# Performance work log

Measured on AMD Instinct MI355X. Metric: run time of the kernel, lower is better.

## Reference

```python
import jax, jax.numpy as jnp
import numpy as np

# Config constants (match init_kwargs)
H = 1024   # hidden_size
F = 4096   # intermediate_size
E = 8      # num_moe_experts
K = 2      # moe_router_topk
S, B = 1024, 2  # seq_len, micro-batch


def setup_inputs() -> dict:
    key = jax.random.key(0)
    ks = jax.random.split(key, 6)
    return {
        "hidden_states": jax.random.normal(ks[0], (S, B, H), jnp.float32),
        "router_w": jax.random.normal(ks[1], (H, E), jnp.float32) * 0.02,
        "w1": jax.random.normal(ks[2], (E, H, F), jnp.float32) * 0.02,
        "b1": jax.random.normal(ks[3], (E, F), jnp.float32) * 0.02,
        "w2": jax.random.normal(ks[4], (E, F, H), jnp.float32) * 0.02,
        "b2": jax.random.normal(ks[5], (E, H), jnp.float32) * 0.02,
    }


def reference(hidden_states, router_w, w1, b1, w2, b2):
    S_, B_, H_ = hidden_states.shape
    x = hidden_states.reshape(-1, H_)                      # [N, H]
    N = x.shape[0]

    # --- TopKRouter (aux_loss routing): topk over logits, softmax over top-k logits ---
    logits = x @ router_w                                  # [N, E]
    top_logits, indices = jax.lax.top_k(logits, K)         # [N, K]
    scores = jax.nn.softmax(top_logits.astype(jnp.float32), axis=-1).astype(logits.dtype)

    # Combine weights [N, E]: scatter top-k scores into expert slots.
    combine = jnp.zeros((N, E), x.dtype).at[jnp.arange(N)[:, None], indices].add(scores)

    # --- Experts: per-expert GPTNeoXMLP (dense over all tokens; math-equivalent
    # to dispatch (token_permutation) + grouped GEMM + scatter_add combine
    # (token_unpermutation) with score weighting for topk>1) ---
    h = jax.nn.gelu(jnp.einsum('nh,ehf->enf', x, w1) + b1[:, None, :], approximate=False)
    y = jnp.einsum('enf,efh->enh', h, w2) + b2[:, None, :]  # [E, N, H]

    out = jnp.einsum('ne,enh->nh', combine, y)              # weighted combine
    return out.reshape(S_, B_, H_)
```

## Files before the change

kernel.cpp:

```cpp
#include <hip/hip_runtime.h>
#include <cmath>


#define H_DIM 1024
#define F_DIM 4096
#define E_NUM 8
#define N_TOK 2048
#define BK 32
#define MAX_SLOTS 5120
#define MAX_MT 40
#define G1_GRID (MAX_MT * 32)
#define G2_GRID (MAX_MT * 8 * 2)
#define CVT_BLKS 2048
#define WCHUNKS (E_NUM * H_DIM * F_DIM / 8)
#define XCHUNKS (N_TOK * H_DIM / 8)

typedef short s16x4 __attribute__((ext_vector_type(4)));
typedef short s16x8 __attribute__((ext_vector_type(8)));
typedef float f32x4 __attribute__((ext_vector_type(4)));
typedef __attribute__((address_space(3))) const unsigned short* lds_us;

__device__ __forceinline__ unsigned short f2bf(float f) {
  unsigned int u = __float_as_uint(f);
  u += 0x7fffu + ((u >> 16) & 1u);
  return (unsigned short)(u >> 16);
}

__device__ __forceinline__ void gload_lds16(const void* g, void* l) {
  __builtin_amdgcn_global_load_lds(
      (const __attribute__((address_space(1))) unsigned int*)g,
      (__attribute__((address_space(3))) unsigned int*)l, 16, 0, 0);
}

__device__ __forceinline__ int xcd_swz(int orig, int nwg) {
  const int cpx = nwg >> 3;
  return (orig & 7) * cpx + (orig >> 3);
}

__device__ __forceinline__ float fast_gelu(float v) {
  const float w = v * (1.0f + 0.044715f * v * v);
  const float t = __expf(-1.5957691216f * w);
  return v / (1.0f + t);
}

template<int OFS>
__device__ __forceinline__ s16x4 trread(lds_us p) {
  s16x4 r;
  asm volatile("ds_read_b64_tr_b16 %0, %1 offset:%2" : "=v"(r) : "v"(p), "i"(OFS));
  return r;
}

__device__ __forceinline__ void ld_b4(lds_us bp, s16x8 bb[4]) {
  s16x4 p0 = trread<0>(bp),    q0 = trread<512>(bp);
  s16x4 p1 = trread<1024>(bp), q1 = trread<1536>(bp);
  s16x4 p2 = trread<2048>(bp), q2 = trread<2560>(bp);
  s16x4 p3 = trread<3072>(bp), q3 = trread<3584>(bp);
  bb[0] = __builtin_shufflevector(p0, q0, 0, 1, 2, 3, 4, 5, 6, 7);
  bb[1] = __builtin_shufflevector(p1, q1, 0, 1, 2, 3, 4, 5, 6, 7);
  bb[2] = __builtin_shufflevector(p2, q2, 0, 1, 2, 3, 4, 5, 6, 7);
  bb[3] = __builtin_shufflevector(p3, q3, 0, 1, 2, 3, 4, 5, 6, 7);
}

__device__ __forceinline__ void cvt_stream(const float* __restrict__ in,
                                           unsigned short* __restrict__ out,
                                           int blk, int nblk, int nchunks) {
  const int step = nblk * 256;
#pragma unroll 4
  for (int c = blk * 256 + threadIdx.x; c < nchunks; c += step) {
    const size_t i = (size_t)c * 8;
    f32x4 a = *(const f32x4*)(in + i);
    f32x4 b = *(const f32x4*)(in + i + 4);
    s16x8 u;
#pragma unroll
    for (int j = 0; j < 4; ++j) { u[j] = (short)f2bf(a[j]); u[4 + j] = (short)f2bf(b[j]); }
    *(s16x8*)&out[i] = u;
  }
}

__global__ __launch_bounds__(256) void prep_k(
    const float* __restrict__ w1, unsigned short* __restrict__ wbf1,
    const float* __restrict__ w2, unsigned short* __restrict__ wbf2,
    const float* __restrict__ x, unsigned short* __restrict__ xb,
    const float* __restrict__ rw, int* __restrict__ topk_e, float* __restrict__ topk_s) {
  const int b = blockIdx.x;
  const int t = threadIdx.x;
  if (b < CVT_BLKS) { cvt_stream(w1, wbf1, b, CVT_BLKS, WCHUNKS); return; }
  if (b < 2 * CVT_BLKS) { cvt_stream(w2, wbf2, b - CVT_BLKS, CVT_BLKS, WCHUNKS); return; }
  if (b < 2 * CVT_BLKS + 128) { cvt_stream(x, xb, b - 2 * CVT_BLKS, 128, XCHUNKS); return; }
  const int n = (b - 2 * CVT_BLKS - 128) * 4 + (t >> 6);
  const int l = t & 63;
  float part[E_NUM];
#pragma unroll
  for (int e = 0; e < E_NUM; ++e) part[e] = 0.f;
  const float* xr = x + (size_t)n * H_DIM;
  for (int h = l; h < H_DIM; h += 64) {
    const float xv = xr[h];
    const float* rwr = rw + h * E_NUM;
#pragma unroll
    for (int e = 0; e < E_NUM; ++e) part[e] += xv * rwr[e];
  }
#pragma unroll
  for (int e = 0; e < E_NUM; ++e) {
#pragma unroll
    for (int off = 32; off > 0; off >>= 1) part[e] += __shfl_down(part[e], off);
  }
  if (l == 0) {
    float v0 = -3.4e38f, v1 = -3.4e38f;
    int i0 = 0, i1 = 0;
#pragma unroll
    for (int e = 0; e < E_NUM; ++e) {
      float v = part[e];
      if (v > v0) { v1 = v0; i1 = i0; v0 = v; i0 = e; }
      else if (v > v1) { v1 = v; i1 = e; }
    }
    const float e1 = expf(v1 - v0);
    const float inv = 1.f / (1.f + e1);
    topk_e[2 * n] = i0; topk_e[2 * n + 1] = i1;
    topk_s[2 * n] = inv; topk_s[2 * n + 1] = e1 * inv;
  }
}

__global__ __launch_bounds__(256) void scatter_k(
    int* __restrict__ meta, const int* __restrict__ topk_e,
    int* __restrict__ slot_token, int* __restrict__ token_slots) {
  __shared__ int cnt[4][8];
  __shared__ int soff[9];
  __shared__ int scur[8];
  const int t = threadIdx.x;
  const int wv = t >> 6;
  if (t < 32) cnt[t >> 3][t & 7] = 0;
  if (t < 8) scur[t] = 0;
  __syncthreads();
  for (int a = t; a < N_TOK * 2; a += 256)
    atomicAdd(&cnt[wv][topk_e[a]], 1);
  __syncthreads();
  if (t == 0) {
    int acc = 0;
    for (int e = 0; e < E_NUM; ++e) {
      const int c = cnt[0][e] + cnt[1][e] + cnt[2][e] + cnt[3][e];
      soff[e] = acc;
      meta[8 + e] = acc;
      acc += ((c + 127) / 128) * 128;
    }
    soff[8] = acc;
    meta[16] = acc;
  }
  __syncthreads();
  for (int a = t; a < N_TOK * 2; a += 256) {
    const int e = topk_e[a];
    const int pos = atomicAdd(&scur[e], 1);
    const int slot = soff[e] + pos;
    slot_token[slot] = a >> 1;
    token_slots[a] = slot;
  }
}

#define KLANE(l) (((l) >> 3 & 3) * 8 + ((l) >> 5) * 4 + (((l) & 7) >> 1))

__global__ __launch_bounds__(256, 3) void gemm1_f(
    const unsigned short* __restrict__ xb, const unsigned short* __restrict__ wbf1,
    const float* __restrict__ b1, const int* __restrict__ meta,
    const int* __restrict__ slot_token, unsigned short* __restrict__ hbuf) {
  __shared__ __align__(16) unsigned short Al[3 * 4096];
  __shared__ __align__(16) unsigned short Bl[3 * 4096];
  const int total = meta[16];
  const int wgid = xcd_swz(blockIdx.x, G1_GRID);
  const int mt = wgid >> 5, nt = wgid & 31;
  const int m0 = mt * 128;
  if (m0 >= total) return;
  int exp = 0;
#pragma unroll
  for (int e = 1; e < E_NUM; ++e) if (m0 >= meta[8 + e]) exp = e;
  const int n0 = nt * 128;
  const int t = threadIdx.x, w = t >> 6, l = t & 63;
  const int wm = w >> 1, wn = w & 1, lr = l & 15, lg = l >> 4;

  const unsigned short* pA[2];
  const unsigned short* pB[2];
#pragma unroll
  for (int i = 0; i < 2; ++i) {
    const int q = w * 2 + i;
    const int row = q * 16 + (l >> 2);
    int tk = slot_token[m0 + row]; if (tk < 0) tk = 0;
    pA[i] = xb + (size_t)tk * H_DIM + (((l & 3) ^ ((l >> 3) & 3)) << 3);
    pB[i] = wbf1 + (size_t)exp * H_DIM * F_DIM + (size_t)KLANE(l) * F_DIM
            + n0 + q * 16 + (l & 1) * 8;
  }

  const f32x4 fzero = {0.f, 0.f, 0.f, 0.f};
  f32x4 acc[4][4];
#pragma unroll
  for (int a = 0; a < 4; ++a)
#pragma unroll
    for (int b = 0; b < 4; ++b) acc[a][b] = fzero;
  const int fofs = ((lg ^ ((lr >> 1) & 3)) << 3);

#define ISSUE1(Ad, Bd)                                                      \
  _Pragma("unroll") for (int i = 0; i < 2; ++i) {                           \
    gload_lds16(pA[i], (Ad) + (w * 2 + i) * 512); pA[i] += BK;              \
    gload_lds16(pB[i], (Bd) + (w * 2 + i) * 512); pB[i] += (size_t)BK * F_DIM; \
  }
#define MFMA1(Ac, Bc)                                                       \
  {                                                                         \
    lds_us bp = (lds_us)(Bc) + wn * 2048 + l * 4;                           \
    s16x8 af[4], bb[4];                                                     \
    _Pragma("unroll") for (int fm = 0; fm < 4; ++fm)                        \
      af[fm] = *(const s16x8*)&(Ac)[(wm * 64 + fm * 16 + lr) * 32 + fofs];  \
    ld_b4(bp, bb);                                                          \
    asm volatile("s_waitcnt lgkmcnt(0)" ::: "memory");                      \
    __builtin_amdgcn_sched_barrier(0);                                      \
    _Pragma("unroll") for (int fm = 0; fm < 4; ++fm)                        \
      _Pragma("unroll") for (int fn = 0; fn < 4; ++fn)                      \
        acc[fm][fn] = __builtin_amdgcn_mfma_f32_16x16x32_bf16(af[fm], bb[fn], acc[fm][fn], 0, 0, 0); \
  }

  const int NT = H_DIM / BK;
  ISSUE1(Al, Bl)
  ISSUE1(Al + 4096, Bl + 4096)
  int cur = 0;
  for (int kt = 0; kt < NT; ++kt) {
    if (kt + 1 < NT) asm volatile("s_waitcnt vmcnt(4)" ::: "memory");
    else             asm volatile("s_waitcnt vmcnt(0)" ::: "memory");
    __builtin_amdgcn_s_barrier();
    __builtin_amdgcn_sched_barrier(0);
    if (kt + 2 < NT) {
      int ib = cur + 2; if (ib >= 3) ib -= 3;
      ISSUE1(Al + ib * 4096, Bl + ib * 4096)
    }
    MFMA1(Al + cur * 4096, Bl + cur * 4096)
    ++cur; if (cur == 3) cur = 0;
  }

#pragma unroll
  for (int fn = 0; fn < 4; ++fn) {
    const int col = n0 + wn * 64 + fn * 16 + lr;
    const float bias = b1[exp * F_DIM + col];
#pragma unroll
    for (int fm = 0; fm < 4; ++fm) {
      const int rbase = m0 + wm * 64 + fm * 16 + lg * 4;
#pragma unroll
      for (int i = 0; i < 4; ++i) {
        hbuf[(size_t)(rbase + i) * F_DIM + col] = f2bf(fast_gelu(acc[fm][fn][i] + bias));
      }
    }
  }
}

__global__ __launch_bounds__(256, 3) void gemm2_f(
    const unsigned short* __restrict__ hbuf, const unsigned short* __restrict__ wbf2,
    const int* __restrict__ meta, unsigned short* __restrict__ yb) {
  __shared__ __align__(16) unsigned short Al[3 * 4096];
  __shared__ __align__(16) unsigned short Bl[3 * 4096];
  const int total = meta[16];
  const int c = blockIdx.x & 7;
  const int r = blockIdx.x >> 3;
  const int nt = c;
  const int ks = r & 1;
  const int mt = r >> 1;
  const int m0 = mt * 128;
  if (m0 >= total) return;
  int exp = 0;
#pragma unroll
  for (int e = 1; e < E_NUM; ++e) if (m0 >= meta[8 + e]) exp = e;
  const int n0 = nt * 128;
  const int k0 = ks * 2048;
  const int t = threadIdx.x, w = t >> 6, l = t & 63;
  const int wm = w >> 1, wn = w & 1, lr = l & 15, lg = l >> 4;

  const unsigned short* pA[2];
  const unsigned short* pB[2];
#pragma unroll
  for (int i = 0; i < 2; ++i) {
    const int q = w * 2 + i;
    const int row = q * 16 + (l >> 2);
    pA[i] = hbuf + (size_t)(m0 + row) * F_DIM + k0 + (((l & 3) ^ ((l >> 3) & 3)) << 3);
    pB[i] = wbf2 + (size_t)exp * F_DIM * H_DIM + (size_t)(k0 + KLANE(l)) * H_DIM
            + n0 + q * 16 + (l & 1) * 8;
  }

  const f32x4 fzero = {0.f, 0.f, 0.f, 0.f};
  f32x4 acc[4][4];
#pragma unroll
  for (int a = 0; a < 4; ++a)
#pragma unroll
    for (int b = 0; b < 4; ++b) acc[a][b] = fzero;
  const int fofs = ((lg ^ ((lr >> 1) & 3)) << 3);

#define ISSUE2(Ad, Bd)                                                      \
  _Pragma("unroll") for (int i = 0; i < 2; ++i) {                           \
    gload_lds16(pA[i], (Ad) + (w * 2 + i) * 512); pA[i] += BK;              \
    gload_lds16(pB[i], (Bd) + (w * 2 + i) * 512); pB[i] += (size_t)BK * H_DIM; \
  }

  const int NT = 2048 / BK;
  ISSUE2(Al, Bl)
  ISSUE2(Al + 4096, Bl + 4096)
  int cur = 0;
  for (int kt = 0; kt < NT; ++kt) {
    if (kt + 1 < NT) asm volatile("s_waitcnt vmcnt(4)" ::: "memory");
    else             asm volatile("s_waitcnt vmcnt(0)" ::: "memory");
    __builtin_amdgcn_s_barrier();
    __builtin_amdgcn_sched_barrier(0);
    if (kt + 2 < NT) {
      int ib = cur + 2; if (ib >= 3) ib -= 3;
      ISSUE2(Al + ib * 4096, Bl + ib * 4096)
    }
    MFMA1(Al + cur * 4096, Bl + cur * 4096)
    ++cur; if (cur == 3) cur = 0;
  }

  unsigned short* yk = yb + (size_t)ks * MAX_SLOTS * H_DIM;
#pragma unroll
  for (int fn = 0; fn < 4; ++fn) {
    const int col = n0 + wn * 64 + fn * 16 + lr;
#pragma unroll
    for (int fm = 0; fm < 4; ++fm) {
      const int rbase = m0 + wm * 64 + fm * 16 + lg * 4;
#pragma unroll
      for (int i = 0; i < 4; ++i) {
        yk[(size_t)(rbase + i) * H_DIM + col] = f2bf(acc[fm][fn][i]);
      }
    }
  }
}

__global__ __launch_bounds__(256) void combine_k(
    const unsigned short* __restrict__ yb, const float* __restrict__ b2,
    const int* __restrict__ token_slots, const int* __restrict__ topk_e,
    const float* __restrict__ topk_s, float* __restrict__ out) {
  const int tok = blockIdx.x;
  const int c4 = threadIdx.x * 4;
  const int sl0 = token_slots[2 * tok], sl1 = token_slots[2 * tok + 1];
  const float s0 = topk_s[2 * tok], s1 = topk_s[2 * tok + 1];
  const int e0 = topk_e[2 * tok], e1 = topk_e[2 * tok + 1];
  const unsigned short* y1p = yb + (size_t)MAX_SLOTS * H_DIM;
  ushort4 a0 = *(const ushort4*)(yb  + (size_t)sl0 * H_DIM + c4);
  ushort4 a1 = *(const ushort4*)(y1p + (size_t)sl0 * H_DIM + c4);
  ushort4 d0 = *(const ushort4*)(yb  + (size_t)sl1 * H_DIM + c4);
  ushort4 d1 = *(const ushort4*)(y1p + (size_t)sl1 * H_DIM + c4);
  f32x4 ba = *(const f32x4*)(b2 + e0 * H_DIM + c4);
  f32x4 bd = *(const f32x4*)(b2 + e1 * H_DIM + c4);
  const unsigned short* ap0 = &a0.x; const unsigned short* ap1 = &a1.x;
  const unsigned short* dp0 = &d0.x; const unsigned short* dp1 = &d1.x;
  f32x4 o;
#pragma unroll
  for (int j = 0; j < 4; ++j) {
    const float ya = __uint_as_float((unsigned)ap0[j] << 16) + __uint_as_float((unsigned)ap1[j] << 16) + ba[j];
    const float yd = __uint_as_float((unsigned)dp0[j] << 16) + __uint_as_float((unsigned)dp1[j] << 16) + bd[j];
    o[j] = s0 * ya + s1 * yd;
  }
  *(f32x4*)(out + (size_t)tok * H_DIM + c4) = o;
}

extern "C" void kernel_launch(void* const* d_in, const int* in_sizes, int n_in,
                              void* d_out, int out_size, void* d_ws, size_t ws_size,
                              hipStream_t stream) {
  const float* x  = (const float*)d_in[0];
  const float* rw = (const float*)d_in[1];
  const float* w1 = (const float*)d_in[2];
  const float* b1 = (const float*)d_in[3];
  const float* w2 = (const float*)d_in[4];
  const float* b2 = (const float*)d_in[5];
  float* out = (float*)d_out;
  char* ws = (char*)d_ws;

  int*   meta        = (int*)ws;
  int*   topk_e      = (int*)(ws + 4096);
  float* topk_s      = (float*)(ws + 36864);
  int*   slot_token  = (int*)(ws + 69632);
  int*   token_slots = (int*)(ws + 102400);
  unsigned short* xb   = (unsigned short*)(ws + (1ull << 20));
  unsigned short* hbuf = (unsigned short*)(ws + (6ull << 20));
  unsigned short* yb   = (unsigned short*)(ws + (46ull << 20));
  unsigned short* wbf1 = (unsigned short*)(ws + (66ull << 20));
  unsigned short* wbf2 = (unsigned short*)(ws + (130ull << 20));
  yb = (unsigned short*)(ws + (66ull << 20));
  wbf1 = (unsigned short*)(ws + (86ull << 20));
  wbf2 = (unsigned short*)(ws + (110ull << 20));
  wbf2 = (unsigned short*)(ws + (46ull << 20));
  yb   = (unsigned short*)(ws + (110ull << 20));
  wbf1 = (unsigned short*)(ws + (130ull << 20));
  wbf1 = (unsigned short*)(ws + (110ull << 20));
  yb   = wbf1;

  hipMemsetAsync(meta, 0, 256, stream);
  hipMemsetAsync(slot_token, 0xFF, MAX_SLOTS * sizeof(int), stream);

  prep_k<<<2 * CVT_BLKS + 128 + 512, 256, 0, stream>>>(
      w1, wbf1, w2, wbf2, x, xb, rw, topk_e, topk_s);
  scatter_k<<<1, 256, 0, stream>>>(meta, topk_e, slot_token, token_slots);
  gemm1_f<<<G1_GRID, 256, 0, stream>>>(xb, wbf1, b1, meta, slot_token, hbuf);
  gemm2_f<<<G2_GRID, 256, 0, stream>>>(hbuf, wbf2, meta, yb);
  combine_k<<<N_TOK, 256, 0, stream>>>(yb, b2, token_slots, topk_e, topk_s, out);
}
```

Before: 253.5 us.

## Overlap w2 bf16 conversion with gemm1 and use nontemporal conversion loads/stores

Moves the fp32-to-bf16 conversion of w2 out of the prep kernel and into extra blocks appended to the gemm1 launch, so it can run alongside the first expert GEMM instead of in front of it. Conversion loads and stores become nontemporal and the unroll factor rises from 4 to 8. Workspace pointer setup is simplified to the final addresses. The risk is that the conversion blocks compete with gemm1 for bandwidth and CU slots, and nontemporal stores may hurt later cache reuse of the bf16 weights.

```diff
diff --git a/kernel.cpp b/kernel.cpp
--- a/kernel.cpp
+++ b/kernel.cpp
@@ -65,29 +65,27 @@
                                            unsigned short* __restrict__ out,
                                            int blk, int nblk, int nchunks) {
   const int step = nblk * 256;
-#pragma unroll 4
+#pragma unroll 8
   for (int c = blk * 256 + threadIdx.x; c < nchunks; c += step) {
     const size_t i = (size_t)c * 8;
-    f32x4 a = *(const f32x4*)(in + i);
-    f32x4 b = *(const f32x4*)(in + i + 4);
+    f32x4 a = __builtin_nontemporal_load((const f32x4*)(in + i));
+    f32x4 b = __builtin_nontemporal_load((const f32x4*)(in + i + 4));
     s16x8 u;
 #pragma unroll
     for (int j = 0; j < 4; ++j) { u[j] = (short)f2bf(a[j]); u[4 + j] = (short)f2bf(b[j]); }
-    *(s16x8*)&out[i] = u;
+    __builtin_nontemporal_store(u, (s16x8*)&out[i]);
   }
 }
 
 __global__ __launch_bounds__(256) void prep_k(
     const float* __restrict__ w1, unsigned short* __restrict__ wbf1,
-    const float* __restrict__ w2, unsigned short* __restrict__ wbf2,
     const float* __restrict__ x, unsigned short* __restrict__ xb,
     const float* __restrict__ rw, int* __restrict__ topk_e, float* __restrict__ topk_s) {
   const int b = blockIdx.x;
   const int t = threadIdx.x;
   if (b < CVT_BLKS) { cvt_stream(w1, wbf1, b, CVT_BLKS, WCHUNKS); return; }
-  if (b < 2 * CVT_BLKS) { cvt_stream(w2, wbf2, b - CVT_BLKS, CVT_BLKS, WCHUNKS); return; }
-  if (b < 2 * CVT_BLKS + 128) { cvt_stream(x, xb, b - 2 * CVT_BLKS, 128, XCHUNKS); return; }
-  const int n = (b - 2 * CVT_BLKS - 128) * 4 + (t >> 6);
+  if (b < CVT_BLKS + 128) { cvt_stream(x, xb, b - CVT_BLKS, 128, XCHUNKS); return; }
+  const int n = (b - CVT_BLKS - 128) * 4 + (t >> 6);
   const int l = t & 63;
   float part[E_NUM];
 #pragma unroll
@@ -160,9 +158,14 @@
 __global__ __launch_bounds__(256, 3) void gemm1_f(
     const unsigned short* __restrict__ xb, const unsigned short* __restrict__ wbf1,
     const float* __restrict__ b1, const int* __restrict__ meta,
-    const int* __restrict__ slot_token, unsigned short* __restrict__ hbuf) {
+    const int* __restrict__ slot_token, unsigned short* __restrict__ hbuf,
+    const float* __restrict__ w2, unsigned short* __restrict__ wbf2) {
   __shared__ __align__(16) unsigned short Al[3 * 4096];
   __shared__ __align__(16) unsigned short Bl[3 * 4096];
+  if (blockIdx.x >= G1_GRID) {
+    cvt_stream(w2, wbf2, blockIdx.x - G1_GRID, CVT_BLKS, WCHUNKS);
+    return;
+  }
   const int total = meta[16];
   const int wgid = xcd_swz(blockIdx.x, G1_GRID);
   const int mt = wgid >> 5, nt = wgid & 31;
@@ -371,25 +374,16 @@
   int*   token_slots = (int*)(ws + 102400);
   unsigned short* xb   = (unsigned short*)(ws + (1ull << 20));
   unsigned short* hbuf = (unsigned short*)(ws + (6ull << 20));
-  unsigned short* yb   = (unsigned short*)(ws + (46ull << 20));
-  unsigned short* wbf1 = (unsigned short*)(ws + (66ull << 20));
-  unsigned short* wbf2 = (unsigned short*)(ws + (130ull << 20));
-  yb = (unsigned short*)(ws + (66ull << 20));
-  wbf1 = (unsigned short*)(ws + (86ull << 20));
-  wbf2 = (unsigned short*)(ws + (110ull << 20));
-  wbf2 = (unsigned short*)(ws + (46ull << 20));
-  yb   = (unsigned short*)(ws + (110ull << 20));
-  wbf1 = (unsigned short*)(ws + (130ull << 20));
-  wbf1 = (unsigned short*)(ws + (110ull << 20));
-  yb   = wbf1;
+  unsigned short* wbf2 = (unsigned short*)(ws + (46ull << 20));
+  unsigned short* wbf1 = (unsigned short*)(ws + (110ull << 20));
+  unsigned short* yb   = wbf1;
 
   hipMemsetAsync(meta, 0, 256, stream);
   hipMemsetAsync(slot_token, 0xFF, MAX_SLOTS * sizeof(int), stream);
 
-  prep_k<<<2 * CVT_BLKS + 128 + 512, 256, 0, stream>>>(
-      w1, wbf1, w2, wbf2, x, xb, rw, topk_e, topk_s);
+  prep_k<<<CVT_BLKS + 128 + 512, 256, 0, stream>>>(w1, wbf1, x, xb, rw, topk_e, topk_s);
   scatter_k<<<1, 256, 0, stream>>>(meta, topk_e, slot_token, token_slots);
-  gemm1_f<<<G1_GRID, 256, 0, stream>>>(xb, wbf1, b1, meta, slot_token, hbuf);
+  gemm1_f<<<G1_GRID + CVT_BLKS, 256, 0, stream>>>(xb, wbf1, b1, meta, slot_token, hbuf, w2, wbf2);
   gemm2_f<<<G2_GRID, 256, 0, stream>>>(hbuf, wbf2, meta, yb);
   combine_k<<<N_TOK, 256, 0, stream>>>(yb, b2, token_slots, topk_e, topk_s, out);
 }
```

Result: slower. 261.7 us (+3.2%).
